# Kernel optimization log

Hardware: AMD Instinct MI355X
Metric: run time of the kernel (lower is better)

The kernel has to match this reference:

```python
import jax, jax.numpy as jnp
import numpy as np

N, E, IN, H, OUT = 50000, 600000, 256, 128, 40
EPS, GAMMA = 0.1, 0.1  # PyG AntiSymmetricConv defaults


def _build_norm(edge_index, n):
    # GCNConv normalization with added self loops: D^-1/2 (A+I) D^-1/2
    loops = jnp.arange(n, dtype=edge_index.dtype)
    src = jnp.concatenate([edge_index[0], loops])
    dst = jnp.concatenate([edge_index[1], loops])
    deg = jax.ops.segment_sum(jnp.ones(src.shape[0], dtype=jnp.float32), dst, num_segments=n)
    dinv = jnp.where(deg > 0, jax.lax.rsqrt(jnp.maximum(deg, 1e-12)), 0.0)
    return src, dst, dinv[src] * dinv[dst]


def _gcn(x, w, src, dst, norm, n):
    # GCNConv(bias=False): scatter normalized messages to target nodes
    m = (x @ w)[src] * norm[:, None]          # [E+N, d]
    return jax.ops.segment_sum(m, dst, num_segments=n)


def _antisym_conv(x, W, gcn_w, bias, src, dst, norm, num_iters):
    d = W.shape[0]
    aW = W - W.T - GAMMA * jnp.eye(d, dtype=W.dtype)  # antisymmetric weight
    n = x.shape[0]

    def step(h, _):
        upd = jnp.tanh(h @ aW.T + _gcn(h, gcn_w, src, dst, norm, n) + bias)
        return h + EPS * upd, None

    x, _ = jax.lax.scan(step, x, None, length=num_iters)
    return x


def setup_inputs() -> dict:
    key = jax.random.key(0)
    ks = jax.random.split(key, 16)
    s = lambda fan: 1.0 / np.sqrt(fan)
    return {
        "x": jax.random.normal(ks[0], (N, IN), dtype=jnp.float32),
        "edge_index": jax.random.randint(ks[1], (2, E), 0, N, dtype=jnp.int64),
        "w_hid": jax.random.normal(ks[2], (H, IN), dtype=jnp.float32) * s(IN),
        "b_hid": jax.random.normal(ks[3], (H,), dtype=jnp.float32) * s(IN),
        "W_a1": jax.random.normal(ks[4], (H, H), dtype=jnp.float32) * s(H),
        "gcn_w1": jax.random.normal(ks[5], (H, H), dtype=jnp.float32) * s(H),
        "b_a1": jax.random.normal(ks[6], (H,), dtype=jnp.float32) * s(H),
        "w_hid2": jax.random.normal(ks[7], (H // 2, H), dtype=jnp.float32) * s(H),
        "b_hid2": jax.random.normal(ks[8], (H // 2,), dtype=jnp.float32) * s(H),
        "W_a2": jax.random.normal(ks[9], (H // 2, H // 2), dtype=jnp.float32) * s(H // 2),
        "gcn_w2": jax.random.normal(ks[10], (H // 2, H // 2), dtype=jnp.float32) * s(H // 2),
        "b_a2": jax.random.normal(ks[11], (H // 2,), dtype=jnp.float32) * s(H // 2),
        "w_fc": jax.random.normal(ks[12], (OUT, H // 2), dtype=jnp.float32) * s(H // 2),
        "b_fc": jax.random.normal(ks[13], (OUT,), dtype=jnp.float32) * s(H // 2),
    }


def reference(x, edge_index, w_hid, b_hid, W_a1, gcn_w1, b_a1,
              w_hid2, b_hid2, W_a2, gcn_w2, b_a2, w_fc, b_fc):
    n = x.shape[0]
    src, dst, norm = _build_norm(edge_index, n)
    h = jax.nn.leaky_relu(x @ w_hid.T + b_hid)          # dropout is no-op in eval
    h = _antisym_conv(h, W_a1, gcn_w1, b_a1, src, dst, norm, num_iters=3)
    h = jax.nn.leaky_relu(h)
    h = jax.nn.leaky_relu(h @ w_hid2.T + b_hid2)
    h = _antisym_conv(h, W_a2, gcn_w2, b_a2, src, dst, norm, num_iters=1)
    out = h @ w_fc.T + b_fc
    return jax.nn.log_softmax(out, axis=1)
```

## Files before the change

### kernel.cpp

```cpp
#include <hip/hip_runtime.h>
#include <hip/hip_bf16.h>
#include <math.h>

typedef unsigned short u16;
typedef unsigned int   u32;
using short8  = __attribute__((ext_vector_type(8))) short;
using f32x4   = __attribute__((ext_vector_type(4))) float;

static constexpr int NNODE = 50000;
static constexpr int NEDGE = 600000;
static constexpr float EPSC   = 0.1f;
static constexpr float GAMMAC = 0.1f;

static constexpr int NTILE  = (NNODE + 63) / 64;
static constexpr int NSPLIT = NTILE * 2;
static constexpr int XDEG   = 160;
static constexpr int XW     = 64;

static constexpr long long O_DINV   = 0;
static constexpr long long O_DEGI   = 50000;
static constexpr long long O_GCUR   = 100000;
static constexpr long long O_ROWPTR = 100004;
static constexpr long long O_CURSOR = 150004;
static constexpr long long O_ECSR   = 200260;
static constexpr long long O_G1TB   = 1400260;
static constexpr long long O_AW1B   = O_G1TB + 8192;
static constexpr long long O_AW2B   = O_AW1B + 8192;
static constexpr long long O_G2TB   = O_AW2B + 2048;
static constexpr long long O_AGGB   = 3450004;
static constexpr long long O_HB0    = O_AGGB + 3200000;
static constexpr long long O_HB1    = O_HB0  + 3200000;
static constexpr long long O_S0     = O_HB1  + 3200000;
static constexpr long long O_S1     = O_S0   + 1600000;

__device__ __forceinline__ float bf2f(u16 u) {
    return __uint_as_float(((unsigned)u) << 16);
}
__device__ __forceinline__ u16 f2bf(float f) {
    unsigned u = __float_as_uint(f);
    return (u16)((u + 0x7FFFu + ((u >> 16) & 1u)) >> 16);
}
__device__ __forceinline__ short8 cvt8(const float4 a, const float4 b) {
    short8 t;
    t[0]=(short)f2bf(a.x); t[1]=(short)f2bf(a.y); t[2]=(short)f2bf(a.z); t[3]=(short)f2bf(a.w);
    t[4]=(short)f2bf(b.x); t[5]=(short)f2bf(b.y); t[6]=(short)f2bf(b.z); t[7]=(short)f2bf(b.w);
    return t;
}
__device__ __forceinline__ float ftanh(float x) {
    float x2 = fminf(fmaxf(2.f * x, -30.f), 30.f);
    float e = __expf(x2);
    return (e - 1.f) * __builtin_amdgcn_rcpf(e + 1.f);
}
__device__ __forceinline__ u16 pk_fp8(float a, float b) {
    int pk = __builtin_amdgcn_cvt_pk_fp8_f32(a, b, 0, false);
    return (u16)(pk & 0xffff);
}
__device__ __forceinline__ void acc_fp8x4(float* a, u32 v, float w) {
    a[0] += __builtin_amdgcn_cvt_f32_fp8(v, 0) * w;
    a[1] += __builtin_amdgcn_cvt_f32_fp8(v, 1) * w;
    a[2] += __builtin_amdgcn_cvt_f32_fp8(v, 2) * w;
    a[3] += __builtin_amdgcn_cvt_f32_fp8(v, 3) * w;
}

__global__ __launch_bounds__(256) void alloc_kernel(const int* __restrict__ degi,
                                                    float* __restrict__ dinv,
                                                    int* __restrict__ rowptr,
                                                    int* __restrict__ cursor,
                                                    int* __restrict__ gcur) {
    int i = blockIdx.x * 256 + threadIdx.x;
    if (i >= NNODE) return;
    int d = degi[i];
    dinv[i] = rsqrtf(1.0f + (float)d);
    int pos = atomicAdd(gcur, d);
    rowptr[i] = pos;
    cursor[i] = pos;
}
__global__ __launch_bounds__(256) void fill_kernel(const int* __restrict__ ei,
                                                   const float* __restrict__ dinv,
                                                   int* __restrict__ cursor,
                                                   int2* __restrict__ ecsr) {
    int e = blockIdx.x * 256 + threadIdx.x;
    if (e >= NEDGE) return;
    int s = ei[e], d = ei[NEDGE + e];
    int pos = atomicAdd(&cursor[d], 1);
    int2 v;
    v.x = s;
    v.y = __float_as_int(dinv[s]);
    ecsr[pos] = v;
}

__global__ __launch_bounds__(256, 6) void xgemm(
    const float* __restrict__ x, const float* __restrict__ w_hid,
    const float* __restrict__ bias,
    u16* __restrict__ outB, u16* __restrict__ outB8,
    const int* __restrict__ ei, int* __restrict__ degi,
    const float* __restrict__ W_a1, const float* __restrict__ gcn1,
    const float* __restrict__ W_a2, const float* __restrict__ gcn2,
    float* __restrict__ ws)
{
    if (blockIdx.x >= NSPLIT) {
        int rb = blockIdx.x - NSPLIT;
        if (rb < XDEG) {
            for (int e = rb * 256 + threadIdx.x; e < NEDGE; e += XDEG * 256)
                atomicAdd(&degi[ei[NEDGE + e]], 1);
        } else {
            u16* g1t = (u16*)(ws + O_G1TB);
            u16* aw1 = (u16*)(ws + O_AW1B);
            u16* aw2 = (u16*)(ws + O_AW2B);
            u16* g2t = (u16*)(ws + O_G2TB);
            for (int j0 = (rb - XDEG) * 256 + threadIdx.x; j0 < 40960; j0 += XW * 256) {
                int j = j0;
                if (j < 16384) { int r=j>>7, c=j&127; g1t[j] = f2bf(gcn1[c*128+r]); }
                else { j -= 16384;
                if (j < 16384) { int r=j>>7, c=j&127;
                    aw1[j] = f2bf(W_a1[r*128+c] - W_a1[c*128+r] - (r==c?GAMMAC:0.f)); }
                else { j -= 16384;
                if (j < 4096)  { int r=j>>6, c=j&63;
                    aw2[j] = f2bf(W_a2[r*64+c] - W_a2[c*64+r] - (r==c?GAMMAC:0.f)); }
                else { j -= 4096; int r=j>>6, c=j&63; g2t[j] = f2bf(gcn2[c*64+r]); } } }
            }
        }
        return;
    }

    constexpr int P = 72, CW = 65;
    __shared__ __align__(16) char smem[9216];
    u16*   bl   = (u16*)smem;
    float* accL = (float*)smem;
    const int wave = threadIdx.x >> 6, lane = threadIdx.x & 63;
    const int m = lane & 15, q = lane >> 4;
    const int tile = blockIdx.x >> 1, nh = blockIdx.x & 1;
    const int rowbase = tile * 64 + wave * 16;
    const int row = rowbase + m;
    const bool rok = row < NNODE;
    const short8 z8 = {0,0,0,0,0,0,0,0};

    short8 af[8];
    {
        const float* apf = x + (long long)row * 256;
        #pragma unroll
        for (int k = 0; k < 8; ++k) {
            short8 t = z8;
            if (rok) {
                const float4* p = (const float4*)(apf + (k * 4 + q) * 8);
                t = cvt8(p[0], p[1]);
            }
            af[k] = t;
        }
    }

    f32x4 acc[4];
    #pragma unroll
    for (int j = 0; j < 4; ++j) acc[j] = (f32x4){0.f,0.f,0.f,0.f};

    #pragma unroll
    for (int ch = 0; ch < 4; ++ch) {
        if (ch) __syncthreads();
        for (int t = threadIdx.x; t < 512; t += 256) {
            int r = t >> 3, c = t & 7;
            const float4* pw = (const float4*)&w_hid[(long long)(nh*64 + r) * 256 + ch*64 + c*8];
            *(short8*)&bl[r * P + c * 8] = cvt8(pw[0], pw[1]);
        }
        __syncthreads();
        #pragma unroll
        for (int j = 0; j < 4; ++j)
            #pragma unroll
            for (int kk = 0; kk < 2; ++kk) {
                short8 b_ = *(const short8*)&bl[(j*16 + m) * P + kk*32 + q*8];
                acc[j] = __builtin_amdgcn_mfma_f32_16x16x32_bf16(af[ch*2 + kk], b_, acc[j], 0, 0, 0);
            }
    }

    const int hw = lane >> 5;
    const int c0 = (lane & 31) * 2;
    float2 bv = {bias[nh*64 + c0], bias[nh*64 + c0 + 1]};
    #pragma unroll
    for (int p = 0; p < 2; ++p) {
        __syncthreads();
        if ((wave >> 1) == p) {
            int lr = (wave & 1) * 16;
            #pragma unroll
            for (int j = 0; j < 4; ++j)
                #pragma unroll
                for (int r = 0; r < 4; ++r)
                    accL[(lr + q*4 + r) * CW + j*16 + m] = acc[j][r];
        }
        __syncthreads();
        if ((wave >> 1) == p) {
            int lr = (wave & 1) * 16;
            #pragma unroll
            for (int rl8 = 0; rl8 < 8; ++rl8) {
                int rl = hw * 8 + rl8;
                int rowD = rowbase + rl;
                if (rowD >= NNODE) continue;
                float2 v = *(const float2*)&accL[(lr + rl) * CW + c0];
                v.x += bv.x; v.y += bv.y;
                v.x = v.x > 0.f ? v.x : 0.01f * v.x;
                v.y = v.y > 0.f ? v.y : 0.01f * v.y;
                long long o = (long long)rowD * 128 + nh*64 + c0;
                ushort2 ob; ob.x = f2bf(v.x); ob.y = f2bf(v.y);
                *(ushort2*)&outB[o] = ob;
                outB8[o >> 1] = pk_fp8(v.x, v.y);
            }
        }
    }
}

template<int HD>
__global__ __launch_bounds__(256) void gather_kernel(
    const int* __restrict__ rowptr, const int* __restrict__ degi,
    const int2* __restrict__ ecsr, const float* __restrict__ dinv,
    const u32* __restrict__ g8, u16* __restrict__ aggB)
{
    int node = (blockIdx.x * 256 + threadIdx.x) >> 6;
    int lane = threadIdx.x & 63;
    if (node >= NNODE) return;
    const int qr = lane >> 4, l4 = lane & 15;
    const int r0 = rowptr[node];
    const int r1 = r0 + degi[node];
    const float dn = dinv[node];
    constexpr int EL = (HD == 128) ? 8 : 4;

    float a[EL];
    #pragma unroll
    for (int i = 0; i < EL; ++i) a[i] = 0.f;
    if (qr == 0) {
        if (HD == 128) {
            uint2 gv = ((const uint2*)g8)[(long long)node * 16 + l4];
            acc_fp8x4(a, gv.x, dn);
            acc_fp8x4(a + 4, gv.y, dn);
        } else {
            u32 gv = g8[(long long)node * 16 + l4];
            acc_fp8x4(a, gv, dn);
        }
    }

    for (int base = r0; base < r1; base += 64) {
        int idx = base + lane;
        int cs = 0; float cw = 0.f;
        if (idx < r1) { int2 ev = ecsr[idx]; cs = ev.x; cw = __int_as_float(ev.y); }
        int cnt = min(64, r1 - base);
        for (int j = 0; j < cnt; j += 16) {
            #pragma unroll
            for (int u = 0; u < 4; ++u) {
                int jj = j + u * 4 + qr;
                int   s = __shfl(cs, jj);
                float w = __shfl(cw, jj);
                if (HD == 128) {
                    uint2 gv = ((const uint2*)g8)[(long long)s * 16 + l4];
                    acc_fp8x4(a, gv.x, w);
                    acc_fp8x4(a + 4, gv.y, w);
                } else {
                    u32 gv = g8[(long long)s * 16 + l4];
                    acc_fp8x4(a, gv, w);
                }
            }
        }
    }

    #pragma unroll
    for (int i = 0; i < EL; ++i) {
        a[i] += __shfl_xor(a[i], 16);
        a[i] += __shfl_xor(a[i], 32);
    }
    if (HD == 128) {
        float v0 = (qr == 0) ? a[0] : (qr == 1) ? a[2] : (qr == 2) ? a[4] : a[6];
        float v1 = (qr == 0) ? a[1] : (qr == 1) ? a[3] : (qr == 2) ? a[5] : a[7];
        v0 *= dn; v1 *= dn;
        long long o = (long long)node * 128 + l4 * 8 + qr * 2;
        ushort2 ob; ob.x = f2bf(v0); ob.y = f2bf(v1);
        *(ushort2*)&aggB[o] = ob;
    } else {
        float v = (qr == 0) ? a[0] : (qr == 1) ? a[1] : (qr == 2) ? a[2] : a[3];
        aggB[(long long)node * 64 + l4 * 4 + qr] = f2bf(v * dn);
    }
}

__global__ __launch_bounds__(256, 6) void convs(
    const u16* __restrict__ hA, const u16* __restrict__ gA,
    const u16* __restrict__ BtW, const u16* __restrict__ BtG,
    const float* __restrict__ bias,
    u16* __restrict__ outB, u16* __restrict__ outB8)
{
    constexpr int K = 128, P = 72, CW = 65;
    __shared__ __align__(16) char smem[9216];
    u16*   bl   = (u16*)smem;
    float* accL = (float*)smem;
    const int wave = threadIdx.x >> 6, lane = threadIdx.x & 63;
    const int m = lane & 15, q = lane >> 4;
    const int tile = blockIdx.x >> 1, nh = blockIdx.x & 1;
    const int rowbase = tile * 64 + wave * 16;
    const int row = rowbase + m;
    const bool rok = row < NNODE;
    const short8 z8 = {0,0,0,0,0,0,0,0};

    short8 af1[4], af2[4];
    {
        const short8* ap1 = (const short8*)(hA + (long long)row * K);
        const short8* ap2 = (const short8*)(gA + (long long)row * K);
        #pragma unroll
        for (int k = 0; k < 4; ++k) {
            af1[k] = rok ? ap1[k * 4 + q] : z8;
            af2[k] = rok ? ap2[k * 4 + q] : z8;
        }
    }

    f32x4 acc[4];
    #pragma unroll
    for (int j = 0; j < 4; ++j) acc[j] = (f32x4){0.f,0.f,0.f,0.f};

    #pragma unroll
    for (int ph = 0; ph < 4; ++ph) {
        const int pass = ph >> 1, ch = ph & 1;
        const u16* Bsrc = pass ? BtG : BtW;
        if (ph) __syncthreads();
        for (int t = threadIdx.x; t < 512; t += 256) {
            int r = t >> 3, c = t & 7;
            *(short8*)&bl[r * P + c * 8] =
                *(const short8*)&Bsrc[(long long)(nh*64 + r) * K + ch*64 + c*8];
        }
        __syncthreads();
        #pragma unroll
        for (int j = 0; j < 4; ++j)
            #pragma unroll
            for (int kk = 0; kk < 2; ++kk) {
                short8 b_ = *(const short8*)&bl[(j*16 + m) * P + kk*32 + q*8];
                acc[j] = __builtin_amdgcn_mfma_f32_16x16x32_bf16(
                    pass ? af2[2*ch + kk] : af1[2*ch + kk], b_, acc[j], 0, 0, 0);
            }
    }

    const int hw = lane >> 5;
    const int c0 = (lane & 31) * 2;
    float2 bv = {bias[nh*64 + c0], bias[nh*64 + c0 + 1]};
    #pragma unroll
    for (int p = 0; p < 2; ++p) {
        __syncthreads();
        if ((wave >> 1) == p) {
            int lr = (wave & 1) * 16;
            #pragma unroll
            for (int j = 0; j < 4; ++j)
                #pragma unroll
                for (int r = 0; r < 4; ++r)
                    accL[(lr + q*4 + r) * CW + j*16 + m] = acc[j][r];
        }
        __syncthreads();
        if ((wave >> 1) == p) {
            int lr = (wave & 1) * 16;
            #pragma unroll
            for (int rl8 = 0; rl8 < 8; ++rl8) {
                int rl = hw * 8 + rl8;
                int rowD = rowbase + rl;
                if (rowD >= NNODE) continue;
                float2 v = *(const float2*)&accL[(lr + rl) * CW + c0];
                long long o = (long long)rowD * 128 + nh*64 + c0;
                ushort2 hh = *(const ushort2*)&hA[o];
                float n0 = bf2f(hh.x) + EPSC * ftanh(v.x + bv.x);
                float n1 = bf2f(hh.y) + EPSC * ftanh(v.y + bv.y);
                ushort2 ob; ob.x = f2bf(n0); ob.y = f2bf(n1);
                *(ushort2*)&outB[o] = ob;
                outB8[o >> 1] = pk_fp8(n0, n1);
            }
        }
    }
}

__global__ __launch_bounds__(256, 4) void convt(
    const u16* __restrict__ hA, const u16* __restrict__ gA,
    const u16* __restrict__ BtW, const u16* __restrict__ BtG,
    const float* __restrict__ bias,
    u16* __restrict__ outB, u16* __restrict__ outB8,
    const float* __restrict__ w2f, const float* __restrict__ b2)
{
    constexpr int K = 128, P = 72, CW = 129, PH = 136;
    __shared__ __align__(16) char smem[18432];
    u16*   bl   = (u16*)smem;
    float* accL = (float*)smem;
    const int wave = threadIdx.x >> 6, lane = threadIdx.x & 63;
    const int m = lane & 15, q = lane >> 4;
    const int rowbase = blockIdx.x * 64 + wave * 16;
    const int row = rowbase + m;
    const bool rok = row < NNODE;
    const short8 z8 = {0,0,0,0,0,0,0,0};

    short8 af1[4], af2[4];
    {
        const short8* ap1 = (const short8*)(hA + (long long)row * K);
        const short8* ap2 = (const short8*)(gA + (long long)row * K);
        #pragma unroll
        for (int k = 0; k < 4; ++k) {
            af1[k] = rok ? ap1[k * 4 + q] : z8;
            af2[k] = rok ? ap2[k * 4 + q] : z8;
        }
    }

    f32x4 acc[8];
    #pragma unroll
    for (int j = 0; j < 8; ++j) acc[j] = (f32x4){0.f,0.f,0.f,0.f};

    #pragma unroll
    for (int ph = 0; ph < 4; ++ph) {
        const int pass = ph >> 1, ch = ph & 1;
        const u16* Bsrc = pass ? BtG : BtW;
        if (ph) __syncthreads();
        for (int t = threadIdx.x; t < 1024; t += 256) {
            int r = t >> 3, c = t & 7;
            *(short8*)&bl[r * P + c * 8] =
                *(const short8*)&Bsrc[(long long)r * K + ch*64 + c*8];
        }
        __syncthreads();
        #pragma unroll
        for (int j = 0; j < 8; ++j)
            #pragma unroll
            for (int kk = 0; kk < 2; ++kk) {
                short8 b_ = *(const short8*)&bl[(j*16 + m) * P + kk*32 + q*8];
                acc[j] = __builtin_amdgcn_mfma_f32_16x16x32_bf16(
                    pass ? af2[2*ch + kk] : af1[2*ch + kk], b_, acc[j], 0, 0, 0);
            }
    }

    const int c0 = lane * 2;
    u32 hv[16];
    {
        float2 bv = {bias[c0], bias[c0 + 1]};
        #pragma unroll
        for (int p = 0; p < 2; ++p) {
            __syncthreads();
            if ((wave >> 1) == p) {
                int lr = (wave & 1) * 16;
                #pragma unroll
                for (int j = 0; j < 8; ++j)
                    #pragma unroll
                    for (int r = 0; r < 4; ++r)
                        accL[(lr + q*4 + r) * CW + j*16 + m] = acc[j][r];
            }
            __syncthreads();
            if ((wave >> 1) == p) {
                int lr = (wave & 1) * 16;
                #pragma unroll
                for (int rl = 0; rl < 16; ++rl) {
                    int rowD = rowbase + rl;
                    float n0 = 0.f, n1 = 0.f;
                    if (rowD < NNODE) {
                        float2 v = *(const float2*)&accL[(lr + rl) * CW + c0];
                        long long o = (long long)rowD * K + c0;
                        ushort2 hh = *(const ushort2*)&hA[o];
                        n0 = bf2f(hh.x) + EPSC * ftanh(v.x + bv.x);
                        n1 = bf2f(hh.y) + EPSC * ftanh(v.y + bv.y);
                        n0 = n0 > 0.f ? n0 : 0.01f * n0;
                        n1 = n1 > 0.f ? n1 : 0.01f * n1;
                    }
                    hv[rl] = (u32)f2bf(n0) | ((u32)f2bf(n1) << 16);
                }
            }
        }
    }

    __syncthreads();
    #pragma unroll
    for (int rl = 0; rl < 16; ++rl)
        *(u32*)&bl[(wave*16 + rl) * PH + c0] = hv[rl];
    __syncthreads();
    short8 af3[4];
    #pragma unroll
    for (int k = 0; k < 4; ++k)
        af3[k] = *(const short8*)&bl[(wave*16 + m) * PH + k*32 + q*8];

    f32x4 acc2[4];
    #pragma unroll
    for (int j = 0; j < 4; ++j) acc2[j] = (f32x4){0.f,0.f,0.f,0.f};
    #pragma unroll
    for (int ch = 0; ch < 2; ++ch) {
        __syncthreads();
        for (int t = threadIdx.x; t < 512; t += 256) {
            int r = t >> 3, c = t & 7;
            const float4* pw = (const float4*)&w2f[(long long)r * K + ch*64 + c*8];
            *(short8*)&bl[r * P + c * 8] = cvt8(pw[0], pw[1]);
        }
        __syncthreads();
        #pragma unroll
        for (int j = 0; j < 4; ++j)
            #pragma unroll
            for (int kk = 0; kk < 2; ++kk) {
                short8 b_ = *(const short8*)&bl[(j*16 + m) * P + kk*32 + q*8];
                acc2[j] = __builtin_amdgcn_mfma_f32_16x16x32_bf16(af3[2*ch + kk], b_, acc2[j], 0, 0, 0);
            }
    }

    constexpr int CW2 = 65;
    const int hw = lane >> 5;
    const int c2 = (lane & 31) * 2;
    float2 bv2 = {b2[c2], b2[c2 + 1]};
    #pragma unroll
    for (int p = 0; p < 2; ++p) {
        __syncthreads();
        if ((wave >> 1) == p) {
            int lr = (wave & 1) * 16;
            #pragma unroll
            for (int j = 0; j < 4; ++j)
                #pragma unroll
                for (int r = 0; r < 4; ++r)
                    accL[(lr + q*4 + r) * CW2 + j*16 + m] = acc2[j][r];
        }
        __syncthreads();
        if ((wave >> 1) == p) {
            int lr = (wave & 1) * 16;
            #pragma unroll
            for (int rl8 = 0; rl8 < 8; ++rl8) {
                int rl = hw * 8 + rl8;
                int rowD = rowbase + rl;
                if (rowD >= NNODE) continue;
                float2 v = *(const float2*)&accL[(lr + rl) * CW2 + c2];
                v.x += bv2.x; v.y += bv2.y;
                v.x = v.x > 0.f ? v.x : 0.01f * v.x;
                v.y = v.y > 0.f ? v.y : 0.01f * v.y;
                long long o = (long long)rowD * 64 + c2;
                ushort2 ob; ob.x = f2bf(v.x); ob.y = f2bf(v.y);
                *(ushort2*)&outB[o] = ob;
                outB8[o >> 1] = pk_fp8(v.x, v.y);
            }
        }
    }
}

__global__ __launch_bounds__(256, 4) void conv2fc(
    const u16* __restrict__ hA,
    const u16* __restrict__ gA,
    const u16* __restrict__ BtW, const u16* __restrict__ BtG,
    const float* __restrict__ bias,
    const float* __restrict__ wfc, const float* __restrict__ bfc,
    float* __restrict__ outF)
{
    constexpr int K = 64, NT = 4, KS = 2, P = 72, CW = 65;
    constexpr int R1 = 64 * CW * 4;
    __shared__ __align__(16) char smem[R1 + 64 * P * 2];
    u16*   bl   = (u16*)smem;
    float* accL = (float*)smem;
    u16*   aggT = (u16*)(smem + R1);
    const int wave = threadIdx.x >> 6, lane = threadIdx.x & 63;
    const int m = lane & 15, q = lane >> 4;
    const int rowbase = blockIdx.x * 64 + wave * 16;
    const int row = rowbase + m;
    const bool rok = row < NNODE;
    const short8 z8 = {0,0,0,0,0,0,0,0};

    short8 af1[KS], af2[KS];
    {
        const short8* ap1 = (const short8*)(hA + (long long)row * K);
        const short8* ap2 = (const short8*)(gA + (long long)row * K);
        #pragma unroll
        for (int k = 0; k < KS; ++k) {
            af1[k] = rok ? ap1[k * 4 + q] : z8;
            af2[k] = rok ? ap2[k * 4 + q] : z8;
        }
    }

    f32x4 acc[NT];
    #pragma unroll
    for (int j = 0; j < NT; ++j) acc[j] = (f32x4){0.f,0.f,0.f,0.f};

    #pragma unroll
    for (int pass = 0; pass < 2; ++pass) {
        const u16* Bcur = pass ? BtG : BtW;
        if (pass) __syncthreads();
        for (int t = threadIdx.x; t < 512; t += 256) {
            int r = t >> 3, c = t & 7;
            *(short8*)&bl[r * P + c * 8] = *(const short8*)&Bcur[(long long)r * K + c * 8];
        }
        __syncthreads();
        #pragma unroll
        for (int j = 0; j < NT; ++j)
            #pragma unroll
            for (int k = 0; k < KS; ++k) {
                short8 b_ = *(const short8*)&bl[(j*16 + m) * P + k*32 + q*8];
                acc[j] = __builtin_amdgcn_mfma_f32_16x16x32_bf16(
                    pass ? af2[k] : af1[k], b_, acc[j], 0, 0, 0);
            }
    }

    __syncthreads();
    #pragma unroll
    for (int j = 0; j < NT; ++j)
        #pragma unroll
        for (int r = 0; r < 4; ++r)
            accL[(wave*16 + q*4 + r) * CW + j*16 + m] = acc[j][r];
    __syncthreads();

    {
        const int c0 = lane * 2;
        if (c0 < 64) {
            float2 bv = {bias[c0], bias[c0 + 1]};
            #pragma unroll
            for (int rl = 0; rl < 16; ++rl) {
                int rowD = rowbase + rl;
                float n0 = 0.f, n1 = 0.f;
                if (rowD < NNODE) {
                    float2 v = *(const float2*)&accL[(wave*16 + rl) * CW + c0];
                    long long o = (long long)rowD * 64 + c0;
                    ushort2 hh = *(const ushort2*)&hA[o];
                    n0 = bf2f(hh.x) + EPSC * ftanh(v.x + bv.x);
                    n1 = bf2f(hh.y) + EPSC * ftanh(v.y + bv.y);
                }
                ushort2 ob; ob.x = f2bf(n0); ob.y = f2bf(n1);
                *(ushort2*)&aggT[(wave*16 + rl) * P + c0] = ob;
            }
        }
    }
    __syncthreads();

    short8 af4[KS];
    #pragma unroll
    for (int k = 0; k < KS; ++k)
        af4[k] = *(const short8*)&aggT[(wave*16 + m) * P + k*32 + q*8];

    for (int t = threadIdx.x; t < 384; t += 256) {
        int r = t >> 3, c = t & 7;
        short8 v = z8;
        if (r < 40) {
            const float4* pw = (const float4*)&wfc[(long long)r * K + c * 8];
            v = cvt8(pw[0], pw[1]);
        }
        *(short8*)&bl[r * P + c * 8] = v;
    }
    __syncthreads();

    f32x4 acc3[3];
    #pragma unroll
    for (int j = 0; j < 3; ++j) acc3[j] = (f32x4){0.f,0.f,0.f,0.f};
    #pragma unroll
    for (int j = 0; j < 3; ++j)
        #pragma unroll
        for (int k = 0; k < KS; ++k) {
            short8 b_ = *(const short8*)&bl[(j*16 + m) * P + k*32 + q*8];
            acc3[j] = __builtin_amdgcn_mfma_f32_16x16x32_bf16(af4[k], b_, acc3[j], 0, 0, 0);
        }

    __syncthreads();
    constexpr int CW3 = 49;
    #pragma unroll
    for (int j = 0; j < 3; ++j)
        #pragma unroll
        for (int r = 0; r < 4; ++r)
            accL[(wave*16 + q*4 + r) * CW3 + j*16 + m] = acc3[j][r];
    __syncthreads();

    float mrow = 0.f, lrow = 0.f;
    if (lane < 16) {
        const float* rp = &accL[(wave*16 + lane) * CW3];
        float mx = -1e30f;
        for (int c = 0; c < 40; ++c) mx = fmaxf(mx, rp[c] + bfc[c]);
        float s = 0.f;
        for (int c = 0; c < 40; ++c) s += expf(rp[c] + bfc[c] - mx);
        mrow = mx; lrow = logf(s);
    }
    for (int rl = 0; rl < 16; ++rl) {
        float mm = __shfl(mrow, rl);
        float ll = __shfl(lrow, rl);
        int rowD = rowbase + rl;
        if (rowD < NNODE && lane < 40) {
            float v = accL[(wave*16 + rl) * CW3 + lane] + bfc[lane];
            outF[(long long)rowD * 40 + lane] = v - mm - ll;
        }
    }
}

extern "C" void kernel_launch(void* const* d_in, const int* in_sizes, int n_in,
                              void* d_out, int out_size, void* d_ws, size_t ws_size,
                              hipStream_t stream) {
    const float* x     = (const float*)d_in[0];
    const int*   ei    = (const int*)d_in[1];
    const float* w_hid = (const float*)d_in[2];
    const float* b_hid = (const float*)d_in[3];
    const float* W_a1  = (const float*)d_in[4];
    const float* gcn1  = (const float*)d_in[5];
    const float* b_a1  = (const float*)d_in[6];
    const float* w2    = (const float*)d_in[7];
    const float* b2    = (const float*)d_in[8];
    const float* W_a2  = (const float*)d_in[9];
    const float* gcn2  = (const float*)d_in[10];
    const float* b_a2  = (const float*)d_in[11];
    const float* wfc   = (const float*)d_in[12];
    const float* bfc   = (const float*)d_in[13];
    float* ws = (float*)d_ws;
    float* out = (float*)d_out;

    float* dinv   = ws + O_DINV;
    int*   degi   = (int*)(ws + O_DEGI);
    int*   gcur   = (int*)(ws + O_GCUR);
    int*   rowptr = (int*)(ws + O_ROWPTR);
    int*   cursor = (int*)(ws + O_CURSOR);
    int2*  ecsr   = (int2*)(ws + O_ECSR);
    u16* g1tB = (u16*)(ws + O_G1TB);
    u16* aw1B = (u16*)(ws + O_AW1B);
    u16* aw2B = (u16*)(ws + O_AW2B);
    u16* g2tB = (u16*)(ws + O_G2TB);
    u16* aggB = (u16*)(ws + O_AGGB);
    u16* hB0  = (u16*)(ws + O_HB0);
    u16* hB1  = (u16*)(ws + O_HB1);
    u16* s0   = (u16*)(ws + O_S0);
    u16* s1   = (u16*)(ws + O_S1);

    hipMemsetAsync((char*)d_ws + (size_t)O_DEGI * 4, 0, (NNODE + 1) * 4, stream);

    xgemm<<<NSPLIT + XDEG + XW, 256, 0, stream>>>(
        x, w_hid, b_hid, hB0, s0, ei, degi, W_a1, gcn1, W_a2, gcn2, ws);

    const int nNodeB = (NNODE + 255) / 256;
    alloc_kernel<<<nNodeB, 256, 0, stream>>>(degi, dinv, rowptr, cursor, gcur);
    fill_kernel<<<(NEDGE + 255) / 256, 256, 0, stream>>>(ei, dinv, cursor, ecsr);

    const int gatherBlocks = (NNODE * 64 + 255) / 256;

    gather_kernel<128><<<gatherBlocks, 256, 0, stream>>>(
        rowptr, degi, ecsr, dinv, (const u32*)s0, aggB);
    convs<<<NSPLIT, 256, 0, stream>>>(hB0, aggB, aw1B, g1tB, b_a1, hB1, s1);
    gather_kernel<128><<<gatherBlocks, 256, 0, stream>>>(
        rowptr, degi, ecsr, dinv, (const u32*)s1, aggB);
    convs<<<NSPLIT, 256, 0, stream>>>(hB1, aggB, aw1B, g1tB, b_a1, hB0, s0);
    gather_kernel<128><<<gatherBlocks, 256, 0, stream>>>(
        rowptr, degi, ecsr, dinv, (const u32*)s0, aggB);
    convt<<<NTILE, 256, 0, stream>>>(hB0, aggB, aw1B, g1tB, b_a1, hB1, s1, w2, b2);

    gather_kernel<64><<<gatherBlocks, 256, 0, stream>>>(
        rowptr, degi, ecsr, dinv, (const u32*)s1, aggB);
    conv2fc<<<NTILE, 256, 0, stream>>>(hB1, aggB, aw2B, g2tB, b_a2, wfc, bfc, out);
}
```

Baseline: 379.9 us.

## Remap xgemm/convs blocks to 32 rows by full 128 columns with per-wave epilogue

Changes the block decomposition in xgemm and convs from 64-row tiles split into two column halves to 32-row tiles covering all 128 output columns, with waves split between row halves and column halves. Each block now stages the full weight slice in doubled shared memory, so every A row fragment is loaded by one block instead of two. The epilogue writes each wave's accumulators to its own LDS region, which replaces the two serialized store/read phases and their barriers. In exchange each block loads twice as many weight rows per chunk and uses twice the LDS, which can reduce occupancy.

```diff
diff --git a/kernel.cpp b/kernel.cpp
--- a/kernel.cpp
+++ b/kernel.cpp
@@ -12,10 +12,10 @@
 static constexpr float EPSC   = 0.1f;
 static constexpr float GAMMAC = 0.1f;
 
-static constexpr int NTILE  = (NNODE + 63) / 64;
-static constexpr int NSPLIT = NTILE * 2;
-static constexpr int XDEG   = 160;
-static constexpr int XW     = 64;
+static constexpr int NTILE = (NNODE + 63) / 64;
+static constexpr int NT32  = (NNODE + 31) / 32;
+static constexpr int XDEG  = 160;
+static constexpr int XW    = 64;
 
 static constexpr long long O_DINV   = 0;
 static constexpr long long O_DEGI   = 50000;
@@ -98,8 +98,8 @@
     const float* __restrict__ W_a2, const float* __restrict__ gcn2,
     float* __restrict__ ws)
 {
-    if (blockIdx.x >= NSPLIT) {
-        int rb = blockIdx.x - NSPLIT;
+    if (blockIdx.x >= NT32) {
+        int rb = blockIdx.x - NT32;
         if (rb < XDEG) {
             for (int e = rb * 256 + threadIdx.x; e < NEDGE; e += XDEG * 256)
                 atomicAdd(&degi[ei[NEDGE + e]], 1);
@@ -123,14 +123,13 @@
         return;
     }
 
-    constexpr int P = 72, CW = 65;
-    __shared__ __align__(16) char smem[9216];
-    u16*   bl   = (u16*)smem;
-    float* accL = (float*)smem;
+    constexpr int P = 72;
+    __shared__ __align__(16) char smem[18432];
+    u16* bl = (u16*)smem;
     const int wave = threadIdx.x >> 6, lane = threadIdx.x & 63;
     const int m = lane & 15, q = lane >> 4;
-    const int tile = blockIdx.x >> 1, nh = blockIdx.x & 1;
-    const int rowbase = tile * 64 + wave * 16;
+    const int nh = wave >> 1;
+    const int rowbase = blockIdx.x * 32 + (wave & 1) * 16;
     const int row = rowbase + m;
     const bool rok = row < NNODE;
     const short8 z8 = {0,0,0,0,0,0,0,0};
@@ -156,9 +155,9 @@
     #pragma unroll
     for (int ch = 0; ch < 4; ++ch) {
         if (ch) __syncthreads();
-        for (int t = threadIdx.x; t < 512; t += 256) {
+        for (int t = threadIdx.x; t < 1024; t += 256) {
             int r = t >> 3, c = t & 7;
-            const float4* pw = (const float4*)&w_hid[(long long)(nh*64 + r) * 256 + ch*64 + c*8];
+            const float4* pw = (const float4*)&w_hid[(long long)r * 256 + ch*64 + c*8];
             *(short8*)&bl[r * P + c * 8] = cvt8(pw[0], pw[1]);
         }
         __syncthreads();
@@ -166,43 +165,35 @@
         for (int j = 0; j < 4; ++j)
             #pragma unroll
             for (int kk = 0; kk < 2; ++kk) {
-                short8 b_ = *(const short8*)&bl[(j*16 + m) * P + kk*32 + q*8];
+                short8 b_ = *(const short8*)&bl[(nh*64 + j*16 + m) * P + kk*32 + q*8];
                 acc[j] = __builtin_amdgcn_mfma_f32_16x16x32_bf16(af[ch*2 + kk], b_, acc[j], 0, 0, 0);
             }
     }
+
+    __syncthreads();
+    float* accW = (float*)smem + wave * 16 * 65;
+    #pragma unroll
+    for (int j = 0; j < 4; ++j)
+        #pragma unroll
+        for (int r = 0; r < 4; ++r)
+            accW[(q*4 + r) * 65 + j*16 + m] = acc[j][r];
 
     const int hw = lane >> 5;
     const int c0 = (lane & 31) * 2;
     float2 bv = {bias[nh*64 + c0], bias[nh*64 + c0 + 1]};
     #pragma unroll
-    for (int p = 0; p < 2; ++p) {
-        __syncthreads();
-        if ((wave >> 1) == p) {
-            int lr = (wave & 1) * 16;
-            #pragma unroll
-            for (int j = 0; j < 4; ++j)
-                #pragma unroll
-                for (int r = 0; r < 4; ++r)
-                    accL[(lr + q*4 + r) * CW + j*16 + m] = acc[j][r];
-        }
-        __syncthreads();
-        if ((wave >> 1) == p) {
-            int lr = (wave & 1) * 16;
-            #pragma unroll
-            for (int rl8 = 0; rl8 < 8; ++rl8) {
-                int rl = hw * 8 + rl8;
-                int rowD = rowbase + rl;
-                if (rowD >= NNODE) continue;
-                float2 v = *(const float2*)&accL[(lr + rl) * CW + c0];
-                v.x += bv.x; v.y += bv.y;
-                v.x = v.x > 0.f ? v.x : 0.01f * v.x;
-                v.y = v.y > 0.f ? v.y : 0.01f * v.y;
-                long long o = (long long)rowD * 128 + nh*64 + c0;
-                ushort2 ob; ob.x = f2bf(v.x); ob.y = f2bf(v.y);
-                *(ushort2*)&outB[o] = ob;
-                outB8[o >> 1] = pk_fp8(v.x, v.y);
-            }
-        }
+    for (int rl8 = 0; rl8 < 8; ++rl8) {
+        int rl = hw * 8 + rl8;
+        int rowD = rowbase + rl;
+        if (rowD >= NNODE) continue;
+        float2 v = *(const float2*)&accW[rl * 65 + c0];
+        v.x += bv.x; v.y += bv.y;
+        v.x = v.x > 0.f ? v.x : 0.01f * v.x;
+        v.y = v.y > 0.f ? v.y : 0.01f * v.y;
+        long long o = (long long)rowD * 128 + nh*64 + c0;
+        ushort2 ob; ob.x = f2bf(v.x); ob.y = f2bf(v.y);
+        *(ushort2*)&outB[o] = ob;
+        outB8[o >> 1] = pk_fp8(v.x, v.y);
     }
 }
 
@@ -282,14 +273,13 @@
     const float* __restrict__ bias,
     u16* __restrict__ outB, u16* __restrict__ outB8)
 {
-    constexpr int K = 128, P = 72, CW = 65;
-    __shared__ __align__(16) char smem[9216];
-    u16*   bl   = (u16*)smem;
-    float* accL = (float*)smem;
+    constexpr int K = 128, P = 72;
+    __shared__ __align__(16) char smem[18432];
+    u16* bl = (u16*)smem;
     const int wave = threadIdx.x >> 6, lane = threadIdx.x & 63;
     const int m = lane & 15, q = lane >> 4;
-    const int tile = blockIdx.x >> 1, nh = blockIdx.x & 1;
-    const int rowbase = tile * 64 + wave * 16;
+    const int nh = wave >> 1;
+    const int rowbase = blockIdx.x * 32 + (wave & 1) * 16;
     const int row = rowbase + m;
     const bool rok = row < NNODE;
     const short8 z8 = {0,0,0,0,0,0,0,0};
@@ -314,54 +304,46 @@
         const int pass = ph >> 1, ch = ph & 1;
         const u16* Bsrc = pass ? BtG : BtW;
         if (ph) __syncthreads();
-        for (int t = threadIdx.x; t < 512; t += 256) {
+        for (int t = threadIdx.x; t < 1024; t += 256) {
             int r = t >> 3, c = t & 7;
             *(short8*)&bl[r * P + c * 8] =
-                *(const short8*)&Bsrc[(long long)(nh*64 + r) * K + ch*64 + c*8];
+                *(const short8*)&Bsrc[(long long)r * K + ch*64 + c*8];
         }
         __syncthreads();
         #pragma unroll
         for (int j = 0; j < 4; ++j)
             #pragma unroll
             for (int kk = 0; kk < 2; ++kk) {
-                short8 b_ = *(const short8*)&bl[(j*16 + m) * P + kk*32 + q*8];
+                short8 b_ = *(const short8*)&bl[(nh*64 + j*16 + m) * P + kk*32 + q*8];
                 acc[j] = __builtin_amdgcn_mfma_f32_16x16x32_bf16(
                     pass ? af2[2*ch + kk] : af1[2*ch + kk], b_, acc[j], 0, 0, 0);
             }
     }
+
+    __syncthreads();
+    float* accW = (float*)smem + wave * 16 * 65;
+    #pragma unroll
+    for (int j = 0; j < 4; ++j)
+        #pragma unroll
+        for (int r = 0; r < 4; ++r)
+            accW[(q*4 + r) * 65 + j*16 + m] = acc[j][r];
 
     const int hw = lane >> 5;
     const int c0 = (lane & 31) * 2;
     float2 bv = {bias[nh*64 + c0], bias[nh*64 + c0 + 1]};
     #pragma unroll
-    for (int p = 0; p < 2; ++p) {
-        __syncthreads();
-        if ((wave >> 1) == p) {
-            int lr = (wave & 1) * 16;
-            #pragma unroll
-            for (int j = 0; j < 4; ++j)
-                #pragma unroll
-                for (int r = 0; r < 4; ++r)
-                    accL[(lr + q*4 + r) * CW + j*16 + m] = acc[j][r];
-        }
-        __syncthreads();
-        if ((wave >> 1) == p) {
-            int lr = (wave & 1) * 16;
-            #pragma unroll
-            for (int rl8 = 0; rl8 < 8; ++rl8) {
-                int rl = hw * 8 + rl8;
-                int rowD = rowbase + rl;
-                if (rowD >= NNODE) continue;
-                float2 v = *(const float2*)&accL[(lr + rl) * CW + c0];
-                long long o = (long long)rowD * 128 + nh*64 + c0;
-                ushort2 hh = *(const ushort2*)&hA[o];
-                float n0 = bf2f(hh.x) + EPSC * ftanh(v.x + bv.x);
-                float n1 = bf2f(hh.y) + EPSC * ftanh(v.y + bv.y);
-                ushort2 ob; ob.x = f2bf(n0); ob.y = f2bf(n1);
-                *(ushort2*)&outB[o] = ob;
-                outB8[o >> 1] = pk_fp8(n0, n1);
-            }
-        }
+    for (int rl8 = 0; rl8 < 8; ++rl8) {
+        int rl = hw * 8 + rl8;
+        int rowD = rowbase + rl;
+        if (rowD >= NNODE) continue;
+        float2 v = *(const float2*)&accW[rl * 65 + c0];
+        long long o = (long long)rowD * 128 + nh*64 + c0;
+        ushort2 hh = *(const ushort2*)&hA[o];
+        float n0 = bf2f(hh.x) + EPSC * ftanh(v.x + bv.x);
+        float n1 = bf2f(hh.y) + EPSC * ftanh(v.y + bv.y);
+        ushort2 ob; ob.x = f2bf(n0); ob.y = f2bf(n1);
+        *(ushort2*)&outB[o] = ob;
+        outB8[o >> 1] = pk_fp8(n0, n1);
     }
 }
 
@@ -702,7 +684,7 @@
 
     hipMemsetAsync((char*)d_ws + (size_t)O_DEGI * 4, 0, (NNODE + 1) * 4, stream);
 
-    xgemm<<<NSPLIT + XDEG + XW, 256, 0, stream>>>(
+    xgemm<<<NT32 + XDEG + XW, 256, 0, stream>>>(
         x, w_hid, b_hid, hB0, s0, ei, degi, W_a1, gcn1, W_a2, gcn2, ws);
 
     const int nNodeB = (NNODE + 255) / 256;
@@ -713,10 +695,10 @@
 
     gather_kernel<128><<<gatherBlocks, 256, 0, stream>>>(
         rowptr, degi, ecsr, dinv, (const u32*)s0, aggB);
-    convs<<<NSPLIT, 256, 0, stream>>>(hB0, aggB, aw1B, g1tB, b_a1, hB1, s1);
+    convs<<<NT32, 256, 0, stream>>>(hB0, aggB, aw1B, g1tB, b_a1, hB1, s1);
     gather_kernel<128><<<gatherBlocks, 256, 0, stream>>>(
         rowptr, degi, ecsr, dinv, (const u32*)s1, aggB);
-    convs<<<NSPLIT, 256, 0, stream>>>(hB1, aggB, aw1B, g1tB, b_a1, hB0, s0);
+    convs<<<NT32, 256, 0, stream>>>(hB1, aggB, aw1B, g1tB, b_a1, hB0, s0);
     gather_kernel<128><<<gatherBlocks, 256, 0, stream>>>(
         rowptr, degi, ecsr, dinv, (const u32*)s0, aggB);
     convt<<<NTILE, 256, 0, stream>>>(hB0, aggB, aw1B, g1tB, b_a1, hB1, s1, w2, b2);
```

After: 373.0 us. No clear change (-1.8%).
